# Optimization experiments

Measured on AMD Instinct MI355X. Metric: run time of the kernel, lower is better.

The kernel has to match this reference:

```python
import jax, jax.numpy as jnp
import numpy as np

N_NODES = 50000
N_EDGES = 262144
HID = 256
N_CLS = 2


def setup_inputs() -> dict:
    key = jax.random.key(0)
    ks = jax.random.split(key, 6)
    node_repr = jax.random.normal(ks[0], (N_NODES, HID), dtype=jnp.float32)
    src = jax.random.randint(ks[1], (N_EDGES,), 0, N_NODES, dtype=jnp.int64)
    dst = jax.random.randint(ks[2], (N_EDGES,), 0, N_NODES, dtype=jnp.int64)
    # Linear weights stored as (in, out); init ~ torch default scale
    W1 = jax.random.normal(ks[3], (4 * HID, 2 * HID), dtype=jnp.float32) * (1.0 / np.sqrt(4 * HID))
    b1 = jnp.zeros((2 * HID,), dtype=jnp.float32)
    W2 = jax.random.normal(ks[4], (2 * HID, N_CLS), dtype=jnp.float32) * (1.0 / np.sqrt(2 * HID))
    b2 = jnp.zeros((N_CLS,), dtype=jnp.float32)
    return {"node_repr": node_repr, "src": src, "dst": dst,
            "W1": W1, "b1": b1, "W2": W2, "b2": b2}


def reference(node_repr, src, dst, W1, b1, W2, b2):
    h_i = node_repr[src]                      # [E, H] gather
    h_j = node_repr[dst]                      # [E, H] gather
    edge_input = jnp.concatenate(
        [h_i, h_j, jnp.abs(h_i - h_j), h_i * h_j], axis=1)  # [E, 4H]
    h = jax.nn.relu(edge_input @ W1 + b1)     # [E, 2H]; dropout = identity (eval)
    return h @ W2 + b2                        # [E, C]
```

## Files before the change

### kernel.cpp

```cpp
#include <hip/hip_runtime.h>

#define N_NODES 50000
#define E_EDGES 262144

typedef __attribute__((ext_vector_type(8))) short bf16x8;
typedef __attribute__((ext_vector_type(4))) float f32x4;

union V16 { uint4 u; bf16x8 h; };

__device__ __forceinline__ unsigned rne_pack(float a, float b) {
  unsigned ua = __float_as_uint(a); ua += 0x7fffu + ((ua >> 16) & 1u);
  unsigned ub = __float_as_uint(b); ub += 0x7fffu + ((ub >> 16) & 1u);
  return (ua >> 16) | (ub & 0xffff0000u);
}
__device__ __forceinline__ float bflo(unsigned u) { return __uint_as_float(u << 16); }
__device__ __forceinline__ float bfhi(unsigned u) { return __uint_as_float(u & 0xffff0000u); }
__device__ __forceinline__ unsigned perm_pack(float a, float b) {
  return __builtin_amdgcn_perm(__float_as_uint(b), __float_as_uint(a), 0x07060302u);
}
__device__ __forceinline__ void async_gather16(const void* gptr, void* lptr) {
  __builtin_amdgcn_global_load_lds(
      (const __attribute__((address_space(1))) void*)gptr,
      (__attribute__((address_space(3))) void*)lptr, 16, 0, 0);
}

__global__ void cvt_node_kernel(const float* __restrict__ x, unsigned short* __restrict__ y) {
  int i = (blockIdx.x * 256 + threadIdx.x) * 8;
  float4 f0 = *(const float4*)(x + i);
  float4 f1 = *(const float4*)(x + i + 4);
  uint4 o;
  o.x = rne_pack(f0.x, f0.y);
  o.y = rne_pack(f0.z, f0.w);
  o.z = rne_pack(f1.x, f1.y);
  o.w = rne_pack(f1.z, f1.w);
  *(uint4*)(y + i) = o;
}

__global__ void prep_w1pp2_kernel(const float* __restrict__ w1, unsigned short* __restrict__ w1pp2) {
  int t = blockIdx.x * 256 + threadIdx.x;
  int step = t >> 13;
  int rem = t & 8191;
  int sq = rem >> 9;
  int col = rem & 511;
  int s = sq >> 2, qd = sq & 3;
  int k0 = s * 256 + step * 32 + qd * 8;
  float f[8];
#pragma unroll
  for (int i = 0; i < 8; ++i) f[i] = w1[(size_t)(k0 + i) * 512 + col];
  uint4 o;
  o.x = rne_pack(f[0], f[1]);
  o.y = rne_pack(f[2], f[3]);
  o.z = rne_pack(f[4], f[5]);
  o.w = rne_pack(f[6], f[7]);
  *(uint4*)(w1pp2 + (size_t)t * 8) = o;
}

__global__ void init_out_kernel(float* __restrict__ out, const float* __restrict__ b2) {
  int i = blockIdx.x * 256 + threadIdx.x;
  float2 v; v.x = b2[0]; v.y = b2[1];
  *(float2*)(out + (size_t)i * 2) = v;
}

__global__ __launch_bounds__(256) void edge_mlp_kernel(
    const unsigned short* __restrict__ nodeb,
    const unsigned short* __restrict__ w1pp2,
    const int* __restrict__ src,
    const int* __restrict__ dst,
    const float* __restrict__ b1,
    const float* __restrict__ w2,
    float* __restrict__ out) {
  __shared__ char smem[65536];

  const int tid = threadIdx.x;
  const int wid = tid >> 6;
  const int lane = tid & 63;
  const int quad = lane >> 4;
  const int l16 = lane & 15;
  const int bx = blockIdx.x;
  const int xc = bx & 7;
  const int t2 = bx >> 3;
  const int n_half = t2 & 1;
  const int m_idx = (t2 >> 1) * 8 + xc;
  const int row0 = m_idx * 64;
  const int n0 = n_half * 256 + wid * 64;

  const char* nodeB = (const char*)nodeb;
  const char* w1B = (const char*)w1pp2;

  unsigned bOff[4];
#pragma unroll
  for (int s = 0; s < 4; ++s)
    bOff[s] = (unsigned)((s * 4 + quad) * 8192 + (n0 + l16) * 16);
  const char* w1s = w1B;

  const unsigned aXor = (unsigned)(l16 & 7);
  const unsigned aBase = (unsigned)(l16 * 512);

  f32x4 acc[4][4];
#pragma unroll
  for (int mt = 0; mt < 4; ++mt)
#pragma unroll
    for (int nt = 0; nt < 4; ++nt)
      acc[mt][nt] = (f32x4){0.f, 0.f, 0.f, 0.f};

  {
    const int eh = tid >> 5;
    const unsigned wsw = (unsigned)(((tid & 31) ^ (eh & 7)) << 4);
#pragma unroll
    for (int c = 0; c < 8; ++c) {
      int e = c * 8 + eh;
      unsigned so = ((unsigned)src[row0 + e] << 9) + wsw;
      unsigned do_ = ((unsigned)dst[row0 + e] << 9) + wsw;
      async_gather16(nodeB + so, smem + c * 4096 + wid * 1024);
      async_gather16(nodeB + do_, smem + 32768 + c * 4096 + wid * 1024);
    }
  }
  __syncthreads();

#pragma unroll 2
  for (int step = 0; step < 8; ++step) {
    V16 bf[4][4];
#pragma unroll
    for (int s = 0; s < 4; ++s)
#pragma unroll
      for (int nt = 0; nt < 4; ++nt)
        bf[s][nt].u = *(const uint4*)(w1s + bOff[s] + nt * 256);
    const unsigned stq = (unsigned)(step * 4 + quad);
    V16 hi[4], hj[4];
#pragma unroll
    for (int mt = 0; mt < 4; ++mt) {
      unsigned ao = (unsigned)(mt * 16 * 512) + aBase + ((stq ^ aXor) << 4);
      hi[mt].u = *(const uint4*)(smem + ao);
      hj[mt].u = *(const uint4*)(smem + 32768 + ao);
    }
#pragma unroll
    for (int sl = 0; sl < 2; ++sl) {
#pragma unroll
      for (int mt = 0; mt < 4; ++mt) {
        bf16x8 af = (sl == 0) ? hi[mt].h : hj[mt].h;
#pragma unroll
        for (int nt = 0; nt < 4; ++nt)
          acc[mt][nt] = __builtin_amdgcn_mfma_f32_16x16x32_bf16(af, bf[sl][nt].h, acc[mt][nt], 0, 0, 0);
      }
    }
#pragma unroll
    for (int mt = 0; mt < 4; ++mt) {
      const unsigned hw[4] = {hi[mt].u.x, hi[mt].u.y, hi[mt].u.z, hi[mt].u.w};
      const unsigned jw[4] = {hj[mt].u.x, hj[mt].u.y, hj[mt].u.z, hj[mt].u.w};
      unsigned d[4], pr[4];
#pragma unroll
      for (int w = 0; w < 4; ++w) {
        float i0 = bflo(hw[w]), i1 = bfhi(hw[w]);
        float j0 = bflo(jw[w]), j1 = bfhi(jw[w]);
        d[w] = perm_pack(i0 - j0, i1 - j1) & 0x7fff7fffu;
        pr[w] = perm_pack(i0 * j0, i1 * j1);
      }
      V16 a2, a3;
      a2.u = make_uint4(d[0], d[1], d[2], d[3]);
      a3.u = make_uint4(pr[0], pr[1], pr[2], pr[3]);
#pragma unroll
      for (int nt = 0; nt < 4; ++nt)
        acc[mt][nt] = __builtin_amdgcn_mfma_f32_16x16x32_bf16(a2.h, bf[2][nt].h, acc[mt][nt], 0, 0, 0);
#pragma unroll
      for (int nt = 0; nt < 4; ++nt)
        acc[mt][nt] = __builtin_amdgcn_mfma_f32_16x16x32_bf16(a3.h, bf[3][nt].h, acc[mt][nt], 0, 0, 0);
    }
    w1s += 131072;
  }

#pragma unroll
  for (int mt = 0; mt < 4; ++mt) {
    float pc0[4] = {0.f, 0.f, 0.f, 0.f};
    float pc1[4] = {0.f, 0.f, 0.f, 0.f};
#pragma unroll
    for (int nt = 0; nt < 4; ++nt) {
      int gc = n0 + nt * 16 + l16;
      float b1v = b1[gc];
      float w20 = w2[gc * 2 + 0];
      float w21 = w2[gc * 2 + 1];
#pragma unroll
      for (int r = 0; r < 4; ++r) {
        float v = fmaxf(acc[mt][nt][r] + b1v, 0.f);
        pc0[r] = fmaf(v, w20, pc0[r]);
        pc1[r] = fmaf(v, w21, pc1[r]);
      }
    }
#pragma unroll
    for (int r = 0; r < 4; ++r) {
      float s0 = pc0[r], s1 = pc1[r];
#pragma unroll
      for (int off = 1; off < 16; off <<= 1) {
        s0 += __shfl_xor(s0, off);
        s1 += __shfl_xor(s1, off);
      }
      int e = row0 + mt * 16 + quad * 4 + r;
      if (l16 == 0) unsafeAtomicAdd(&out[(size_t)e * 2 + 0], s0);
      if (l16 == 1) unsafeAtomicAdd(&out[(size_t)e * 2 + 1], s1);
    }
  }
}

extern "C" void kernel_launch(void* const* d_in, const int* in_sizes, int n_in,
                              void* d_out, int out_size, void* d_ws, size_t ws_size,
                              hipStream_t stream) {
  const float* node = (const float*)d_in[0];
  const int* src = (const int*)d_in[1];
  const int* dst = (const int*)d_in[2];
  const float* W1 = (const float*)d_in[3];
  const float* b1 = (const float*)d_in[4];
  const float* W2 = (const float*)d_in[5];
  const float* b2 = (const float*)d_in[6];
  float* out = (float*)d_out;

  unsigned short* nodeb = (unsigned short*)d_ws;
  unsigned short* w1pp2 = (unsigned short*)((char*)d_ws + 25600000);

  cvt_node_kernel<<<6250, 256, 0, stream>>>(node, nodeb);
  prep_w1pp2_kernel<<<256, 256, 0, stream>>>(W1, w1pp2);
  init_out_kernel<<<1024, 256, 0, stream>>>(out, b2);
  edge_mlp_kernel<<<8192, 256, 0, stream>>>(nodeb, w1pp2, src, dst, b1, W2, out);
}
```

Measured before the change: 411.7 us.

## Precompute abs-diff and product tiles in LDS and split M across 8 waves

The edge MLP block grows from 256 to 512 threads. Each wave now owns 32 rows instead of 64, so accumulator registers per wave are halved. The |hi-hj| and hi*hj features are computed once per block into two new 32KB LDS regions, instead of being recomputed inside every step by each of the four N-waves. The cost is 128KB of LDS per block, which likely limits occupancy to one block per CU. It also adds an extra barrier and doubles the W1 B-fragment global reads per block, since each of the two M-halves loads the same weights.

```diff
diff --git a/kernel.cpp b/kernel.cpp
--- a/kernel.cpp
+++ b/kernel.cpp
@@ -61,7 +61,7 @@
   *(float2*)(out + (size_t)i * 2) = v;
 }
 
-__global__ __launch_bounds__(256) void edge_mlp_kernel(
+__global__ __launch_bounds__(512) void edge_mlp_kernel(
     const unsigned short* __restrict__ nodeb,
     const unsigned short* __restrict__ w1pp2,
     const int* __restrict__ src,
@@ -69,7 +69,7 @@
     const float* __restrict__ b1,
     const float* __restrict__ w2,
     float* __restrict__ out) {
-  __shared__ char smem[65536];
+  __shared__ char smem[131072];
 
   const int tid = threadIdx.x;
   const int wid = tid >> 6;
@@ -82,7 +82,9 @@
   const int n_half = t2 & 1;
   const int m_idx = (t2 >> 1) * 8 + xc;
   const int row0 = m_idx * 64;
-  const int n0 = n_half * 256 + wid * 64;
+  const int mh = wid >> 2;
+  const int ns = wid & 3;
+  const int n0 = n_half * 256 + ns * 64;
 
   const char* nodeB = (const char*)nodeb;
   const char* w1B = (const char*)w1pp2;
@@ -93,30 +95,52 @@
     bOff[s] = (unsigned)((s * 4 + quad) * 8192 + (n0 + l16) * 16);
   const char* w1s = w1B;
 
-  const unsigned aXor = (unsigned)(l16 & 7);
-  const unsigned aBase = (unsigned)(l16 * 512);
-
-  f32x4 acc[4][4];
-#pragma unroll
-  for (int mt = 0; mt < 4; ++mt)
+  f32x4 acc[2][4];
+#pragma unroll
+  for (int mt = 0; mt < 2; ++mt)
 #pragma unroll
     for (int nt = 0; nt < 4; ++nt)
       acc[mt][nt] = (f32x4){0.f, 0.f, 0.f, 0.f};
 
   {
-    const int eh = tid >> 5;
-    const unsigned wsw = (unsigned)(((tid & 31) ^ (eh & 7)) << 4);
-#pragma unroll
-    for (int c = 0; c < 8; ++c) {
-      int e = c * 8 + eh;
-      unsigned so = ((unsigned)src[row0 + e] << 9) + wsw;
-      unsigned do_ = ((unsigned)dst[row0 + e] << 9) + wsw;
-      async_gather16(nodeB + so, smem + c * 4096 + wid * 1024);
-      async_gather16(nodeB + do_, smem + 32768 + c * 4096 + wid * 1024);
+    const int ehc = tid >> 5;
+    const int wsl = tid & 31;
+#pragma unroll
+    for (int c = 0; c < 4; ++c) {
+      int e = c * 16 + ehc;
+      unsigned uo = (unsigned)((wsl ^ (e & 7)) << 4);
+      unsigned so = ((unsigned)src[row0 + e] << 9) + uo;
+      unsigned dofs = ((unsigned)dst[row0 + e] << 9) + uo;
+      async_gather16(nodeB + so, smem + c * 8192 + wid * 1024);
+      async_gather16(nodeB + dofs, smem + 32768 + c * 8192 + wid * 1024);
     }
   }
   __syncthreads();
 
+#pragma unroll
+  for (int k = 0; k < 4; ++k) {
+    int p = k * 512 + tid;
+    unsigned off = (unsigned)((p >> 5) * 512 + (((p & 31) ^ ((p >> 5) & 7)) << 4));
+    V16 a, b;
+    a.u = *(const uint4*)(smem + off);
+    b.u = *(const uint4*)(smem + 32768 + off);
+    const unsigned hw[4] = {a.u.x, a.u.y, a.u.z, a.u.w};
+    const unsigned jw[4] = {b.u.x, b.u.y, b.u.z, b.u.w};
+    unsigned d[4], pr[4];
+#pragma unroll
+    for (int w = 0; w < 4; ++w) {
+      float i0 = bflo(hw[w]), i1 = bfhi(hw[w]);
+      float j0 = bflo(jw[w]), j1 = bfhi(jw[w]);
+      d[w] = perm_pack(i0 - j0, i1 - j1) & 0x7fff7fffu;
+      pr[w] = perm_pack(i0 * j0, i1 * j1);
+    }
+    *(uint4*)(smem + 65536 + off) = make_uint4(d[0], d[1], d[2], d[3]);
+    *(uint4*)(smem + 98304 + off) = make_uint4(pr[0], pr[1], pr[2], pr[3]);
+  }
+  __syncthreads();
+
+  const unsigned aBase = (unsigned)((mh * 32 + l16) * 512);
+  const unsigned aXor = (unsigned)(l16 & 7);
 #pragma unroll 2
   for (int step = 0; step < 8; ++step) {
     V16 bf[4][4];
@@ -125,51 +149,25 @@
 #pragma unroll
       for (int nt = 0; nt < 4; ++nt)
         bf[s][nt].u = *(const uint4*)(w1s + bOff[s] + nt * 256);
-    const unsigned stq = (unsigned)(step * 4 + quad);
-    V16 hi[4], hj[4];
-#pragma unroll
-    for (int mt = 0; mt < 4; ++mt) {
-      unsigned ao = (unsigned)(mt * 16 * 512) + aBase + ((stq ^ aXor) << 4);
-      hi[mt].u = *(const uint4*)(smem + ao);
-      hj[mt].u = *(const uint4*)(smem + 32768 + ao);
-    }
-#pragma unroll
-    for (int sl = 0; sl < 2; ++sl) {
-#pragma unroll
-      for (int mt = 0; mt < 4; ++mt) {
-        bf16x8 af = (sl == 0) ? hi[mt].h : hj[mt].h;
+    const unsigned sw = (((unsigned)(step * 4 + quad) ^ aXor) << 4);
+    V16 af[2][4];
+#pragma unroll
+    for (int mt = 0; mt < 2; ++mt)
+#pragma unroll
+      for (int s = 0; s < 4; ++s)
+        af[mt][s].u = *(const uint4*)(smem + s * 32768 + aBase + mt * 8192 + sw);
+#pragma unroll
+    for (int s = 0; s < 4; ++s)
+#pragma unroll
+      for (int mt = 0; mt < 2; ++mt)
 #pragma unroll
         for (int nt = 0; nt < 4; ++nt)
-          acc[mt][nt] = __builtin_amdgcn_mfma_f32_16x16x32_bf16(af, bf[sl][nt].h, acc[mt][nt], 0, 0, 0);
-      }
-    }
-#pragma unroll
-    for (int mt = 0; mt < 4; ++mt) {
-      const unsigned hw[4] = {hi[mt].u.x, hi[mt].u.y, hi[mt].u.z, hi[mt].u.w};
-      const unsigned jw[4] = {hj[mt].u.x, hj[mt].u.y, hj[mt].u.z, hj[mt].u.w};
-      unsigned d[4], pr[4];
-#pragma unroll
-      for (int w = 0; w < 4; ++w) {
-        float i0 = bflo(hw[w]), i1 = bfhi(hw[w]);
-        float j0 = bflo(jw[w]), j1 = bfhi(jw[w]);
-        d[w] = perm_pack(i0 - j0, i1 - j1) & 0x7fff7fffu;
-        pr[w] = perm_pack(i0 * j0, i1 * j1);
-      }
-      V16 a2, a3;
-      a2.u = make_uint4(d[0], d[1], d[2], d[3]);
-      a3.u = make_uint4(pr[0], pr[1], pr[2], pr[3]);
-#pragma unroll
-      for (int nt = 0; nt < 4; ++nt)
-        acc[mt][nt] = __builtin_amdgcn_mfma_f32_16x16x32_bf16(a2.h, bf[2][nt].h, acc[mt][nt], 0, 0, 0);
-#pragma unroll
-      for (int nt = 0; nt < 4; ++nt)
-        acc[mt][nt] = __builtin_amdgcn_mfma_f32_16x16x32_bf16(a3.h, bf[3][nt].h, acc[mt][nt], 0, 0, 0);
-    }
+          acc[mt][nt] = __builtin_amdgcn_mfma_f32_16x16x32_bf16(af[mt][s].h, bf[s][nt].h, acc[mt][nt], 0, 0, 0);
     w1s += 131072;
   }
 
 #pragma unroll
-  for (int mt = 0; mt < 4; ++mt) {
+  for (int mt = 0; mt < 2; ++mt) {
     float pc0[4] = {0.f, 0.f, 0.f, 0.f};
     float pc1[4] = {0.f, 0.f, 0.f, 0.f};
 #pragma unroll
@@ -193,7 +191,7 @@
         s0 += __shfl_xor(s0, off);
         s1 += __shfl_xor(s1, off);
       }
-      int e = row0 + mt * 16 + quad * 4 + r;
+      int e = row0 + mh * 32 + mt * 16 + quad * 4 + r;
       if (l16 == 0) unsafeAtomicAdd(&out[(size_t)e * 2 + 0], s0);
       if (l16 == 1) unsafeAtomicAdd(&out[(size_t)e * 2 + 1], s1);
     }
@@ -218,5 +216,5 @@
   cvt_node_kernel<<<6250, 256, 0, stream>>>(node, nodeb);
   prep_w1pp2_kernel<<<256, 256, 0, stream>>>(W1, w1pp2);
   init_out_kernel<<<1024, 256, 0, stream>>>(out, b2);
-  edge_mlp_kernel<<<8192, 256, 0, stream>>>(nodeb, w1pp2, src, dst, b1, W2, out);
-}
+  edge_mlp_kernel<<<8192, 512, 0, stream>>>(nodeb, w1pp2, src, dst, b1, W2, out);
+}
```

Measured after the change: 532.3 us. 29.3% more time.

## Gather node rows directly into registers with smaller per-wave tiles, dropping LDS staging

Applied to the files above, without the earlier changes.

The LDS staging of gathered src/dst node rows via async global-to-LDS loads and the block barrier are removed. Each lane now loads its edge's bf16 row chunk straight from global memory into registers, prefetching the next k-step one iteration ahead. The tiling changes from 4-wave blocks computing 64 edges by 256 columns (each wave 64x64) to 8-wave blocks computing 128 edges by 64 columns (each wave 16x64), with twice as many blocks. This aims to cut LDS use and barrier cost and raise occupancy. In exchange, each W1 fragment load now feeds a quarter as many MFMAs, and node rows are re-gathered by eight column blocks instead of two, which multiplies global and L2 traffic.

```diff
diff --git a/kernel.cpp b/kernel.cpp
--- a/kernel.cpp
+++ b/kernel.cpp
@@ -17,11 +17,6 @@
 __device__ __forceinline__ float bfhi(unsigned u) { return __uint_as_float(u & 0xffff0000u); }
 __device__ __forceinline__ unsigned perm_pack(float a, float b) {
   return __builtin_amdgcn_perm(__float_as_uint(b), __float_as_uint(a), 0x07060302u);
-}
-__device__ __forceinline__ void async_gather16(const void* gptr, void* lptr) {
-  __builtin_amdgcn_global_load_lds(
-      (const __attribute__((address_space(1))) void*)gptr,
-      (__attribute__((address_space(3))) void*)lptr, 16, 0, 0);
 }
 
 __global__ void cvt_node_kernel(const float* __restrict__ x, unsigned short* __restrict__ y) {
@@ -61,7 +56,7 @@
   *(float2*)(out + (size_t)i * 2) = v;
 }
 
-__global__ __launch_bounds__(256) void edge_mlp_kernel(
+__global__ __launch_bounds__(512) void edge_mlp_kernel(
     const unsigned short* __restrict__ nodeb,
     const unsigned short* __restrict__ w1pp2,
     const int* __restrict__ src,
@@ -69,8 +64,6 @@
     const float* __restrict__ b1,
     const float* __restrict__ w2,
     float* __restrict__ out) {
-  __shared__ char smem[65536];
-
   const int tid = threadIdx.x;
   const int wid = tid >> 6;
   const int lane = tid & 63;
@@ -78,14 +71,17 @@
   const int l16 = lane & 15;
   const int bx = blockIdx.x;
   const int xc = bx & 7;
-  const int t2 = bx >> 3;
-  const int n_half = t2 & 1;
-  const int m_idx = (t2 >> 1) * 8 + xc;
-  const int row0 = m_idx * 64;
-  const int n0 = n_half * 256 + wid * 64;
+  const int n_idx = (bx >> 3) & 7;
+  const int m_idx = (bx >> 6) * 8 + xc;
+  const int row0 = m_idx * 128;
+  const int erow = row0 + wid * 16 + l16;
+  const int n0 = n_idx * 64;
 
   const char* nodeB = (const char*)nodeb;
   const char* w1B = (const char*)w1pp2;
+
+  const char* pi = nodeB + ((unsigned)src[erow] << 9) + (unsigned)(quad << 4);
+  const char* pj = nodeB + ((unsigned)dst[erow] << 9) + (unsigned)(quad << 4);
 
   unsigned bOff[4];
 #pragma unroll
@@ -93,29 +89,13 @@
     bOff[s] = (unsigned)((s * 4 + quad) * 8192 + (n0 + l16) * 16);
   const char* w1s = w1B;
 
-  const unsigned aXor = (unsigned)(l16 & 7);
-  const unsigned aBase = (unsigned)(l16 * 512);
+  f32x4 acc[4];
+#pragma unroll
+  for (int nt = 0; nt < 4; ++nt) acc[nt] = (f32x4){0.f, 0.f, 0.f, 0.f};
 
-  f32x4 acc[4][4];
-#pragma unroll
-  for (int mt = 0; mt < 4; ++mt)
-#pragma unroll
-    for (int nt = 0; nt < 4; ++nt)
-      acc[mt][nt] = (f32x4){0.f, 0.f, 0.f, 0.f};
-
-  {
-    const int eh = tid >> 5;
-    const unsigned wsw = (unsigned)(((tid & 31) ^ (eh & 7)) << 4);
-#pragma unroll
-    for (int c = 0; c < 8; ++c) {
-      int e = c * 8 + eh;
-      unsigned so = ((unsigned)src[row0 + e] << 9) + wsw;
-      unsigned do_ = ((unsigned)dst[row0 + e] << 9) + wsw;
-      async_gather16(nodeB + so, smem + c * 4096 + wid * 1024);
-      async_gather16(nodeB + do_, smem + 32768 + c * 4096 + wid * 1024);
-    }
-  }
-  __syncthreads();
+  V16 hiC, hjC;
+  hiC.u = *(const uint4*)pi;
+  hjC.u = *(const uint4*)pj;
 
 #pragma unroll 2
   for (int step = 0; step < 8; ++step) {
@@ -125,51 +105,46 @@
 #pragma unroll
       for (int nt = 0; nt < 4; ++nt)
         bf[s][nt].u = *(const uint4*)(w1s + bOff[s] + nt * 256);
-    const unsigned stq = (unsigned)(step * 4 + quad);
-    V16 hi[4], hj[4];
-#pragma unroll
-    for (int mt = 0; mt < 4; ++mt) {
-      unsigned ao = (unsigned)(mt * 16 * 512) + aBase + ((stq ^ aXor) << 4);
-      hi[mt].u = *(const uint4*)(smem + ao);
-      hj[mt].u = *(const uint4*)(smem + 32768 + ao);
+    V16 hiN, hjN;
+    if (step < 7) {
+      hiN.u = *(const uint4*)(pi + (step + 1) * 64);
+      hjN.u = *(const uint4*)(pj + (step + 1) * 64);
     }
 #pragma unroll
-    for (int sl = 0; sl < 2; ++sl) {
+    for (int nt = 0; nt < 4; ++nt)
+      acc[nt] = __builtin_amdgcn_mfma_f32_16x16x32_bf16(hiC.h, bf[0][nt].h, acc[nt], 0, 0, 0);
 #pragma unroll
-      for (int mt = 0; mt < 4; ++mt) {
-        bf16x8 af = (sl == 0) ? hi[mt].h : hj[mt].h;
-#pragma unroll
-        for (int nt = 0; nt < 4; ++nt)
-          acc[mt][nt] = __builtin_amdgcn_mfma_f32_16x16x32_bf16(af, bf[sl][nt].h, acc[mt][nt], 0, 0, 0);
-      }
-    }
-#pragma unroll
-    for (int mt = 0; mt < 4; ++mt) {
-      const unsigned hw[4] = {hi[mt].u.x, hi[mt].u.y, hi[mt].u.z, hi[mt].u.w};
-      const unsigned jw[4] = {hj[mt].u.x, hj[mt].u.y, hj[mt].u.z, hj[mt].u.w};
+    for (int nt = 0; nt < 4; ++nt)
+      acc[nt] = __builtin_amdgcn_mfma_f32_16x16x32_bf16(hjC.h, bf[1][nt].h, acc[nt], 0, 0, 0);
+    {
+      const unsigned hw[4] = {hiC.u.x, hiC.u.y, hiC.u.z, hiC.u.w};
+      const unsigned jw[4] = {hjC.u.x, hjC.u.y, hjC.u.z, hjC.u.w};
       unsigned d[4], pr[4];
 #pragma unroll
       for (int w = 0; w < 4; ++w) {
-        float i0 = bflo(hw[w]), i1 = bfhi(hw[w]);
-        float j0 = bflo(jw[w]), j1 = bfhi(jw[w]);
-        d[w] = perm_pack(i0 - j0, i1 - j1) & 0x7fff7fffu;
-        pr[w] = perm_pack(i0 * j0, i1 * j1);
+        float2 iv = make_float2(bflo(hw[w]), bfhi(hw[w]));
+        float2 jv = make_float2(bflo(jw[w]), bfhi(jw[w]));
+        float2 dv = make_float2(iv.x - jv.x, iv.y - jv.y);
+        float2 pv = make_float2(iv.x * jv.x, iv.y * jv.y);
+        d[w] = perm_pack(dv.x, dv.y) & 0x7fff7fffu;
+        pr[w] = perm_pack(pv.x, pv.y);
       }
       V16 a2, a3;
       a2.u = make_uint4(d[0], d[1], d[2], d[3]);
       a3.u = make_uint4(pr[0], pr[1], pr[2], pr[3]);
 #pragma unroll
       for (int nt = 0; nt < 4; ++nt)
-        acc[mt][nt] = __builtin_amdgcn_mfma_f32_16x16x32_bf16(a2.h, bf[2][nt].h, acc[mt][nt], 0, 0, 0);
+        acc[nt] = __builtin_amdgcn_mfma_f32_16x16x32_bf16(a2.h, bf[2][nt].h, acc[nt], 0, 0, 0);
 #pragma unroll
       for (int nt = 0; nt < 4; ++nt)
-        acc[mt][nt] = __builtin_amdgcn_mfma_f32_16x16x32_bf16(a3.h, bf[3][nt].h, acc[mt][nt], 0, 0, 0);
+        acc[nt] = __builtin_amdgcn_mfma_f32_16x16x32_bf16(a3.h, bf[3][nt].h, acc[nt], 0, 0, 0);
     }
+    hiC = hiN;
+    hjC = hjN;
     w1s += 131072;
   }
 
-#pragma unroll
-  for (int mt = 0; mt < 4; ++mt) {
+  {
     float pc0[4] = {0.f, 0.f, 0.f, 0.f};
     float pc1[4] = {0.f, 0.f, 0.f, 0.f};
 #pragma unroll
@@ -180,7 +155,7 @@
       float w21 = w2[gc * 2 + 1];
 #pragma unroll
       for (int r = 0; r < 4; ++r) {
-        float v = fmaxf(acc[mt][nt][r] + b1v, 0.f);
+        float v = fmaxf(acc[nt][r] + b1v, 0.f);
         pc0[r] = fmaf(v, w20, pc0[r]);
         pc1[r] = fmaf(v, w21, pc1[r]);
       }
@@ -193,7 +168,7 @@
         s0 += __shfl_xor(s0, off);
         s1 += __shfl_xor(s1, off);
       }
-      int e = row0 + mt * 16 + quad * 4 + r;
+      int e = row0 + wid * 16 + quad * 4 + r;
       if (l16 == 0) unsafeAtomicAdd(&out[(size_t)e * 2 + 0], s0);
       if (l16 == 1) unsafeAtomicAdd(&out[(size_t)e * 2 + 1], s1);
     }
@@ -218,5 +193,5 @@
   cvt_node_kernel<<<6250, 256, 0, stream>>>(node, nodeb);
   prep_w1pp2_kernel<<<256, 256, 0, stream>>>(W1, w1pp2);
   init_out_kernel<<<1024, 256, 0, stream>>>(out, b2);
-  edge_mlp_kernel<<<8192, 256, 0, stream>>>(nodeb, w1pp2, src, dst, b1, W2, out);
+  edge_mlp_kernel<<<16384, 512, 0, stream>>>(nodeb, w1pp2, src, dst, b1, W2, out);
 }
```

New measurement: 844.6 us. 105% more time.

## Use 512-thread blocks with 32-column warp tiles to cut register pressure

Applied to the files above, without the earlier changes.

Doubles the block to 8 wavefronts, each now covering 32 output columns instead of 64. This halves the per-wave accumulator and B-fragment registers, and the launch bounds ask for 4 blocks per CU. The A fragments are now loaded and consumed one row tile at a time, and the step loop is no longer unrolled. The aim is higher occupancy to hide latency. In exchange, each wave reads more shared memory per MFMA, and with 64KB of LDS per block, four resident blocks may not fit.

```diff
diff --git a/kernel.cpp b/kernel.cpp
--- a/kernel.cpp
+++ b/kernel.cpp
@@ -61,7 +61,7 @@
   *(float2*)(out + (size_t)i * 2) = v;
 }
 
-__global__ __launch_bounds__(256) void edge_mlp_kernel(
+__global__ __launch_bounds__(512, 4) void edge_mlp_kernel(
     const unsigned short* __restrict__ nodeb,
     const unsigned short* __restrict__ w1pp2,
     const int* __restrict__ src,
@@ -78,11 +78,10 @@
   const int l16 = lane & 15;
   const int bx = blockIdx.x;
   const int xc = bx & 7;
-  const int t2 = bx >> 3;
-  const int n_half = t2 & 1;
-  const int m_idx = (t2 >> 1) * 8 + xc;
+  const int n_half = (bx >> 3) & 1;
+  const int m_idx = (bx >> 4) * 8 + xc;
   const int row0 = m_idx * 64;
-  const int n0 = n_half * 256 + wid * 64;
+  const int n0 = n_half * 256 + wid * 32;
 
   const char* nodeB = (const char*)nodeb;
   const char* w1B = (const char*)w1pp2;
@@ -93,60 +92,53 @@
     bOff[s] = (unsigned)((s * 4 + quad) * 8192 + (n0 + l16) * 16);
   const char* w1s = w1B;
 
-  const unsigned aXor = (unsigned)(l16 & 7);
-  const unsigned aBase = (unsigned)(l16 * 512);
-
-  f32x4 acc[4][4];
+  f32x4 acc[4][2];
 #pragma unroll
   for (int mt = 0; mt < 4; ++mt)
 #pragma unroll
-    for (int nt = 0; nt < 4; ++nt)
+    for (int nt = 0; nt < 2; ++nt)
       acc[mt][nt] = (f32x4){0.f, 0.f, 0.f, 0.f};
 
   {
     const int eh = tid >> 5;
-    const unsigned wsw = (unsigned)(((tid & 31) ^ (eh & 7)) << 4);
-#pragma unroll
-    for (int c = 0; c < 8; ++c) {
-      int e = c * 8 + eh;
-      unsigned so = ((unsigned)src[row0 + e] << 9) + wsw;
-      unsigned do_ = ((unsigned)dst[row0 + e] << 9) + wsw;
-      async_gather16(nodeB + so, smem + c * 4096 + wid * 1024);
-      async_gather16(nodeB + do_, smem + 32768 + c * 4096 + wid * 1024);
+    const int wsl = tid & 31;
+#pragma unroll
+    for (int c = 0; c < 4; ++c) {
+      int e = c * 16 + eh;
+      unsigned uo = (unsigned)((wsl ^ (e & 7)) << 4);
+      unsigned so = ((unsigned)src[row0 + e] << 9) + uo;
+      unsigned dofs = ((unsigned)dst[row0 + e] << 9) + uo;
+      async_gather16(nodeB + so, smem + c * 8192 + wid * 1024);
+      async_gather16(nodeB + dofs, smem + 32768 + c * 8192 + wid * 1024);
     }
   }
   __syncthreads();
 
-#pragma unroll 2
+  const unsigned aBase = (unsigned)(l16 * 512);
+  const unsigned aXor = (unsigned)(l16 & 7);
+#pragma unroll 1
   for (int step = 0; step < 8; ++step) {
-    V16 bf[4][4];
+    V16 bf[4][2];
 #pragma unroll
     for (int s = 0; s < 4; ++s)
 #pragma unroll
-      for (int nt = 0; nt < 4; ++nt)
+      for (int nt = 0; nt < 2; ++nt)
         bf[s][nt].u = *(const uint4*)(w1s + bOff[s] + nt * 256);
-    const unsigned stq = (unsigned)(step * 4 + quad);
-    V16 hi[4], hj[4];
+    const unsigned sw = (((unsigned)(step * 4 + quad) ^ aXor) << 4);
 #pragma unroll
     for (int mt = 0; mt < 4; ++mt) {
-      unsigned ao = (unsigned)(mt * 16 * 512) + aBase + ((stq ^ aXor) << 4);
-      hi[mt].u = *(const uint4*)(smem + ao);
-      hj[mt].u = *(const uint4*)(smem + 32768 + ao);
-    }
-#pragma unroll
-    for (int sl = 0; sl < 2; ++sl) {
-#pragma unroll
-      for (int mt = 0; mt < 4; ++mt) {
-        bf16x8 af = (sl == 0) ? hi[mt].h : hj[mt].h;
-#pragma unroll
-        for (int nt = 0; nt < 4; ++nt)
-          acc[mt][nt] = __builtin_amdgcn_mfma_f32_16x16x32_bf16(af, bf[sl][nt].h, acc[mt][nt], 0, 0, 0);
-      }
-    }
-#pragma unroll
-    for (int mt = 0; mt < 4; ++mt) {
-      const unsigned hw[4] = {hi[mt].u.x, hi[mt].u.y, hi[mt].u.z, hi[mt].u.w};
-      const unsigned jw[4] = {hj[mt].u.x, hj[mt].u.y, hj[mt].u.z, hj[mt].u.w};
+      V16 hi, hj;
+      unsigned ao = (unsigned)(mt * 8192) + aBase + sw;
+      hi.u = *(const uint4*)(smem + ao);
+      hj.u = *(const uint4*)(smem + 32768 + ao);
+#pragma unroll
+      for (int nt = 0; nt < 2; ++nt)
+        acc[mt][nt] = __builtin_amdgcn_mfma_f32_16x16x32_bf16(hi.h, bf[0][nt].h, acc[mt][nt], 0, 0, 0);
+#pragma unroll
+      for (int nt = 0; nt < 2; ++nt)
+        acc[mt][nt] = __builtin_amdgcn_mfma_f32_16x16x32_bf16(hj.h, bf[1][nt].h, acc[mt][nt], 0, 0, 0);
+      const unsigned hw[4] = {hi.u.x, hi.u.y, hi.u.z, hi.u.w};
+      const unsigned jw[4] = {hj.u.x, hj.u.y, hj.u.z, hj.u.w};
       unsigned d[4], pr[4];
 #pragma unroll
       for (int w = 0; w < 4; ++w) {
@@ -159,10 +151,10 @@
       a2.u = make_uint4(d[0], d[1], d[2], d[3]);
       a3.u = make_uint4(pr[0], pr[1], pr[2], pr[3]);
 #pragma unroll
-      for (int nt = 0; nt < 4; ++nt)
+      for (int nt = 0; nt < 2; ++nt)
         acc[mt][nt] = __builtin_amdgcn_mfma_f32_16x16x32_bf16(a2.h, bf[2][nt].h, acc[mt][nt], 0, 0, 0);
 #pragma unroll
-      for (int nt = 0; nt < 4; ++nt)
+      for (int nt = 0; nt < 2; ++nt)
         acc[mt][nt] = __builtin_amdgcn_mfma_f32_16x16x32_bf16(a3.h, bf[3][nt].h, acc[mt][nt], 0, 0, 0);
     }
     w1s += 131072;
@@ -173,7 +165,7 @@
     float pc0[4] = {0.f, 0.f, 0.f, 0.f};
     float pc1[4] = {0.f, 0.f, 0.f, 0.f};
 #pragma unroll
-    for (int nt = 0; nt < 4; ++nt) {
+    for (int nt = 0; nt < 2; ++nt) {
       int gc = n0 + nt * 16 + l16;
       float b1v = b1[gc];
       float w20 = w2[gc * 2 + 0];
@@ -218,5 +210,5 @@
   cvt_node_kernel<<<6250, 256, 0, stream>>>(node, nodeb);
   prep_w1pp2_kernel<<<256, 256, 0, stream>>>(W1, w1pp2);
   init_out_kernel<<<1024, 256, 0, stream>>>(out, b2);
-  edge_mlp_kernel<<<8192, 256, 0, stream>>>(nodeb, w1pp2, src, dst, b1, W2, out);
-}
+  edge_mlp_kernel<<<8192, 512, 0, stream>>>(nodeb, w1pp2, src, dst, b1, W2, out);
+}
```

After: 493.1 us. 19.8% more time.
